# Optimization experiments

Hardware: AMD Instinct MI355X
Metric: run time of the kernel (lower is better)

Reference implementation:

```python
import jax, jax.numpy as jnp
import numpy as np

TOP_K = 2
AUX_COEF = 0.001


def setup_inputs() -> dict:
    key = jax.random.key(0)
    ks = jax.random.split(key, 5)
    B, S, H, I, E = 4, 2048, 1024, 4096, 8
    return {
        "hidden_states": jax.random.normal(ks[0], (B, S, H), dtype=jnp.float32),
        "router_w": jax.random.normal(ks[1], (H, E), dtype=jnp.float32) * 0.02,
        "w_gate": jax.random.normal(ks[2], (E, H, I), dtype=jnp.float32) * 0.02,
        "w_up": jax.random.normal(ks[3], (E, H, I), dtype=jnp.float32) * 0.02,
        "w_down": jax.random.normal(ks[4], (E, I, H), dtype=jnp.float32) * 0.02,
    }


def reference(hidden_states, router_w, w_gate, w_up, w_down):
    B, S, H = hidden_states.shape
    E = router_w.shape[1]
    x = jnp.clip(hidden_states, -10.0, 10.0)          # [B,S,H]
    xf = x.reshape(-1, H)                              # [T,H]
    T = xf.shape[0]

    # --- token-choice router (fp32) ---
    logits = xf.astype(jnp.float32) @ router_w         # [T,E]
    z_loss = jnp.mean(jax.nn.logsumexp(logits, axis=-1) ** 2)
    probs = jax.nn.softmax(logits, axis=-1)            # [T,E]
    top_w, top_i = jax.lax.top_k(probs, TOP_K)         # [T,K]
    top_w = top_w / jnp.sum(top_w, axis=-1, keepdims=True)
    # load-balance loss: aux * E * sum_e f_e * P_e
    assign = jax.nn.one_hot(top_i, E, dtype=jnp.float32).sum(axis=1)  # [T,E]
    frac_tokens = assign.mean(axis=0) / TOP_K
    mean_probs = probs.mean(axis=0)
    lb_loss = AUX_COEF * E * jnp.sum(frac_tokens * mean_probs)

    # --- dense per-expert SwiGLU MLP, then gather selected outputs ---
    expert_outs = []
    for e in range(E):  # small fixed loop over experts
        gate = xf @ w_gate[e]                          # [T,I]
        up = xf @ w_up[e]                              # [T,I]
        expert_outs.append((jax.nn.silu(gate) * up) @ w_down[e])  # [T,H]
    outs = jnp.stack(expert_outs, axis=0)              # [E,T,H]

    gathered = outs[top_i, jnp.arange(T)[:, None], :]  # [T,K,H]
    out = jnp.einsum("tk,tkh->th", top_w.astype(x.dtype), gathered)
    out = jnp.clip(out, -10.0, 10.0).reshape(B, S, H)
    return out, lb_loss, z_loss
```

## Files before the change

kernel.cpp:

```cpp
#include <hip/hip_runtime.h>
#include <stdint.h>

#define TOKENS 8192
#define HDIM 1024
#define IDIM 4096
#define NEXP 8
#define MPAD 17408
#define MTILES 136

typedef float f32x4 __attribute__((ext_vector_type(4)));
typedef __bf16 bf16x8 __attribute__((ext_vector_type(8)));
typedef uint32_t u32x4 __attribute__((ext_vector_type(4)));

static __device__ __forceinline__ uint16_t f2bf(float f) {
  uint32_t u = __builtin_bit_cast(uint32_t, f);
  return (uint16_t)((u + 0x7fffu + ((u >> 16) & 1u)) >> 16);
}
static __device__ __forceinline__ uint32_t pack2(float a, float b) {
  return (uint32_t)f2bf(a) | ((uint32_t)f2bf(b) << 16);
}
static __device__ __forceinline__ float bf2f(uint32_t h) {
  return __builtin_bit_cast(float, h << 16);
}
#define SWZ4(r) (((r) >> 1) & 3u)
static __device__ __forceinline__ void load_lds16(const void* g, void* l) {
  __builtin_amdgcn_global_load_lds(
      (const __attribute__((address_space(1))) uint32_t*)(uintptr_t)g,
      (__attribute__((address_space(3))) uint32_t*)(uintptr_t)l, 16, 0, 0);
}
static __device__ __forceinline__ bf16x8 rdfrag(const char* base, uint32_t row, uint32_t g) {
  return *(const bf16x8*)(base + row * 64 + ((g ^ SWZ4(row)) * 16));
}
static __device__ __forceinline__ void nt_store4(void* p, u32x4 v) {
  __builtin_nontemporal_store(v, (u32x4*)p);
}
#define WAITV(n) asm volatile("s_waitcnt vmcnt(" #n ")" ::: "memory")
#define WAITL0 asm volatile("s_waitcnt lgkmcnt(0)" ::: "memory")
#define BAR __builtin_amdgcn_s_barrier()
#define SCHEDB __builtin_amdgcn_sched_barrier(0)

__global__ __launch_bounds__(256) void router_kernel(
    const float* __restrict__ x, const float* __restrict__ rw,
    uint16_t* __restrict__ xb, float2* __restrict__ topw, int2* __restrict__ tope,
    int* __restrict__ cnt_slots, float* __restrict__ psum_slots, float* __restrict__ zsum_slots) {
  const int tid = threadIdx.x;
  const int lane = tid & 63, wid = tid >> 6;
  const int t = blockIdx.x * 4 + wid;

  const float* xrow = x + (size_t)t * HDIM + lane * 16;
  float xc[16];
#pragma unroll
  for (int i = 0; i < 4; ++i) {
    float4 v = *(const float4*)(xrow + i * 4);
    xc[i * 4 + 0] = fminf(fmaxf(v.x, -10.f), 10.f);
    xc[i * 4 + 1] = fminf(fmaxf(v.y, -10.f), 10.f);
    xc[i * 4 + 2] = fminf(fmaxf(v.z, -10.f), 10.f);
    xc[i * 4 + 3] = fminf(fmaxf(v.w, -10.f), 10.f);
  }
  uint4 o0, o1;
  o0.x = pack2(xc[0], xc[1]);   o0.y = pack2(xc[2], xc[3]);
  o0.z = pack2(xc[4], xc[5]);   o0.w = pack2(xc[6], xc[7]);
  o1.x = pack2(xc[8], xc[9]);   o1.y = pack2(xc[10], xc[11]);
  o1.z = pack2(xc[12], xc[13]); o1.w = pack2(xc[14], xc[15]);
  uint4* dst = (uint4*)(xb + (size_t)t * HDIM + lane * 16);
  dst[0] = o0; dst[1] = o1;

  float acc[8];
#pragma unroll
  for (int e = 0; e < 8; ++e) acc[e] = 0.f;
  const float* rwp = rw + (size_t)(lane * 16) * NEXP;
#pragma unroll
  for (int i = 0; i < 16; ++i) {
    float xi = xc[i];
    float4 a = *(const float4*)(rwp + i * 8);
    float4 b = *(const float4*)(rwp + i * 8 + 4);
    acc[0] += xi * a.x; acc[1] += xi * a.y; acc[2] += xi * a.z; acc[3] += xi * a.w;
    acc[4] += xi * b.x; acc[5] += xi * b.y; acc[6] += xi * b.z; acc[7] += xi * b.w;
  }
#pragma unroll
  for (int s = 1; s < 64; s <<= 1) {
#pragma unroll
    for (int e = 0; e < 8; ++e) acc[e] += __shfl_xor(acc[e], s);
  }

  __shared__ float sp[8]; __shared__ int sc[8]; __shared__ float sz;
  if (tid < 8) { sp[tid] = 0.f; sc[tid] = 0; }
  if (tid == 0) sz = 0.f;
  __syncthreads();

  if (lane == 0) {
    float mx = acc[0];
#pragma unroll
    for (int e = 1; e < 8; ++e) mx = fmaxf(mx, acc[e]);
    float p[8]; float s = 0.f;
#pragma unroll
    for (int e = 0; e < 8; ++e) { p[e] = expf(acc[e] - mx); s += p[e]; }
    float inv = 1.f / s;
#pragma unroll
    for (int e = 0; e < 8; ++e) p[e] *= inv;
    float lse = mx + logf(s);
    int e0 = 0; float b0 = p[0];
#pragma unroll
    for (int e = 1; e < 8; ++e) if (p[e] > b0) { b0 = p[e]; e0 = e; }
    int e1 = (e0 == 0) ? 1 : 0; float b1 = (e0 == 0) ? p[1] : p[0];
#pragma unroll
    for (int e = 0; e < 8; ++e) if (e != e0 && p[e] > b1) { b1 = p[e]; e1 = e; }
    float wn = 1.f / (b0 + b1);
    topw[t] = make_float2(b0 * wn, b1 * wn);
    tope[t] = make_int2(e0, e1);
#pragma unroll
    for (int e = 0; e < 8; ++e) atomicAdd(&sp[e], p[e]);
    atomicAdd(&sc[e0], 1); atomicAdd(&sc[e1], 1);
    atomicAdd(&sz, lse * lse);
  }
  __syncthreads();
  int slot = blockIdx.x & 63;
  if (tid < 8) {
    atomicAdd(&cnt_slots[slot * 8 + tid], sc[tid]);
    atomicAdd(&psum_slots[slot * 8 + tid], sp[tid]);
  }
  if (tid == 0) atomicAdd(&zsum_slots[slot], sz);
}

__global__ void scan_kernel(const int* __restrict__ cnt_slots,
                            const float* __restrict__ psum_slots,
                            const float* __restrict__ zsum_slots,
                            int* __restrict__ seg, int* __restrict__ fill_cnt,
                            float* __restrict__ out_sc) {
  const int tid = threadIdx.x;
  __shared__ int c[8]; __shared__ float ps[8];
  if (tid < 8) {
    int s = 0; float f = 0.f;
    for (int k = 0; k < 64; ++k) { s += cnt_slots[k * 8 + tid]; f += psum_slots[k * 8 + tid]; }
    c[tid] = s; ps[tid] = f; fill_cnt[tid] = 0;
  }
  __syncthreads();
  if (tid == 0) {
    int off = 0;
    for (int e = 0; e < 8; ++e) { seg[e] = off; off += (c[e] + 127) & ~127; }
    seg[8] = off;
    float lb = 0.f;
    for (int e = 0; e < 8; ++e)
      lb += ((float)c[e] / (2.0f * (float)TOKENS)) * (ps[e] / (float)TOKENS);
    lb *= 0.001f * (float)NEXP;
    float z = 0.f;
    for (int k = 0; k < 64; ++k) z += zsum_slots[k];
    out_sc[0] = lb;
    out_sc[1] = z / (float)TOKENS;
  }
}

__global__ __launch_bounds__(256) void fill_kernel(
    const int2* __restrict__ tope, const int* __restrict__ seg,
    int* __restrict__ fill_cnt, int* __restrict__ rowtok) {
  const int t = blockIdx.x * 256 + threadIdx.x;
  const int lane = threadIdx.x & 63;
  const int2 te = tope[t];
#pragma unroll
  for (int k = 0; k < 2; ++k) {
    const int e = k ? te.y : te.x;
    int pos = 0;
    for (int ee = 0; ee < 8; ++ee) {
      unsigned long long mask = __ballot(e == ee);
      if (e == ee) {
        unsigned long long below = mask & ((lane == 0) ? 0ull : (~0ull >> (64 - lane)));
        int nbelow = __popcll(below);
        int leader = __ffsll((unsigned long long)mask) - 1;
        int base = 0;
        if (lane == leader) base = atomicAdd(&fill_cnt[ee], __popcll(mask));
        base = __shfl(base, leader);
        pos = seg[ee] + base + nbelow;
      }
    }
    rowtok[pos] = t * 2 + k;
  }
}

__global__ __launch_bounds__(256) void convert_kernel(
    const float* __restrict__ w_gate, const float* __restrict__ w_up,
    const float* __restrict__ w_down, uint16_t* __restrict__ wgT,
    uint16_t* __restrict__ wuT, uint16_t* __restrict__ wdT) {
  __shared__ uint64_t tt4[4][64][17];
  const int tid = threadIdx.x;
  const int z = blockIdx.y;
  const int bx = blockIdx.x;
  const float* src; uint16_t* dst; int R, C, tr, tq;
  if (z < 16) {
    R = 1024; C = 4096; tr = bx >> 4; tq = bx & 15;
    int e = z & 7;
    src = (z < 8 ? w_gate : w_up) + (size_t)e * 1024 * 4096;
    dst = (z < 8 ? wgT : wuT) + (size_t)e * 1024 * 4096;
  } else {
    R = 4096; C = 1024; tr = bx >> 2; tq = bx & 3;
    int e = z - 16;
    src = w_down + (size_t)e * 4096 * 1024;
    dst = wdT + (size_t)e * 4096 * 1024;
  }
  const int i = tid >> 4, j = tid & 15;
  const float* sb = src + (size_t)(tr * 64 + 4 * i) * C + tq * 256 + 4 * j;
  f32x4 v[4][4];
#pragma unroll
  for (int t4 = 0; t4 < 4; ++t4)
#pragma unroll
    for (int r = 0; r < 4; ++r)
      v[t4][r] = __builtin_nontemporal_load((const f32x4*)(sb + (size_t)r * C + t4 * 64));
#pragma unroll
  for (int t4 = 0; t4 < 4; ++t4)
#pragma unroll
    for (int k = 0; k < 4; ++k)
      tt4[t4][4 * j + k][i] =
          (uint64_t)pack2(v[t4][0][k], v[t4][1][k]) |
          ((uint64_t)pack2(v[t4][2][k], v[t4][3][k]) << 32);
  __syncthreads();
#pragma unroll
  for (int t4 = 0; t4 < 4; ++t4)
#pragma unroll
    for (int it = 0; it < 2; ++it) {
      int idx = it * 256 + tid;
      int c = idx >> 3, h = idx & 7;
      uint64_t a = tt4[t4][c][2 * h], b = tt4[t4][c][2 * h + 1];
      u32x4 w;
      w[0] = (uint32_t)a; w[1] = (uint32_t)(a >> 32);
      w[2] = (uint32_t)b; w[3] = (uint32_t)(b >> 32);
      nt_store4(dst + (size_t)(tq * 256 + t4 * 64 + c) * R + tr * 64 + h * 8, w);
    }
}

static __device__ __forceinline__ int xcd_swz(int b, int nwg) {
  int q = nwg >> 3, r = nwg & 7;
  int xcd = b & 7;
  int base = (xcd < r) ? xcd * (q + 1) : r * (q + 1) + (xcd - r) * q;
  return base + (b >> 3);
}

__global__ __launch_bounds__(256, 2) void gemm1_kernel(
    const uint16_t* __restrict__ xb, const uint16_t* __restrict__ wgT,
    const uint16_t* __restrict__ wuT, const int* __restrict__ rowtok,
    const int* __restrict__ seg, uint16_t* __restrict__ hbuf, int mt0) {
  __shared__ __align__(16) char smem[49152];
  const int tid = threadIdx.x;
  const int lane = tid & 63, wid = tid >> 6;
  const int ct = (int)gridDim.y;
  const int b = (int)(blockIdx.y * gridDim.x + blockIdx.x);
  const int wg_lin = xcd_swz(b, 32 * ct);
  const int iblk = wg_lin / ct;
  const int mrel = wg_lin % ct;
  const int mtile = mt0 + mrel;
  const int row0 = mtile * 128;
  if (row0 >= seg[8]) return;
  int e = 0;
  while (row0 >= seg[e + 1]) ++e;
  const uint16_t* wgp = wgT + (size_t)e * HDIM * IDIM;
  const uint16_t* wup = wuT + (size_t)e * HDIM * IDIM;
  const int icol0 = iblk * 128;

  const uint32_t r0 = (uint32_t)(wid * 32 + (lane >> 2));
  const uint32_t r1 = r0 + 16;
  const uint32_t cc0 = ((lane & 3u) ^ SWZ4(r0)) * 16;
  const uint32_t cc1 = ((lane & 3u) ^ SWZ4(r1)) * 16;
  int rt0 = rowtok[row0 + r0]; int tok0 = (rt0 < 0) ? 0 : (rt0 >> 1);
  int rt1 = rowtok[row0 + r1]; int tok1 = (rt1 < 0) ? 0 : (rt1 >> 1);
  const uintptr_t a0 = (uintptr_t)(xb + (size_t)tok0 * HDIM) + cc0;
  const uintptr_t a1 = (uintptr_t)(xb + (size_t)tok1 * HDIM) + cc1;
  const uintptr_t g0 = (uintptr_t)(wgp + (size_t)(icol0 + r0) * HDIM) + cc0;
  const uintptr_t g1 = (uintptr_t)(wgp + (size_t)(icol0 + r1) * HDIM) + cc1;
  const uintptr_t u0 = (uintptr_t)(wup + (size_t)(icol0 + r0) * HDIM) + cc0;
  const uintptr_t u1 = (uintptr_t)(wup + (size_t)(icol0 + r1) * HDIM) + cc1;
  const uint32_t ldsA = (uint32_t)(wid * 2048);

  f32x4 accg[4][4] = {}; f32x4 accu[4][4] = {};

#define G1_ISSUE(t, buf)                                                        \
  {                                                                             \
    char* B_ = smem + (buf) * 24576;                                            \
    size_t o_ = (size_t)(t) * 64;                                               \
    load_lds16((const void*)(a0 + o_), B_ + ldsA);                              \
    load_lds16((const void*)(a1 + o_), B_ + ldsA + 1024);                       \
    load_lds16((const void*)(g0 + o_), B_ + 8192 + ldsA);                       \
    load_lds16((const void*)(g1 + o_), B_ + 8192 + ldsA + 1024);                \
    load_lds16((const void*)(u0 + o_), B_ + 16384 + ldsA);                      \
    load_lds16((const void*)(u1 + o_), B_ + 16384 + ldsA + 1024);               \
  }

  const uint32_t g = lane >> 4, l15 = lane & 15;
  const uint32_t mrow = (uint32_t)((wid >> 1) * 64) + l15;
  const uint32_t nrow = (uint32_t)((wid & 1) * 64) + l15;

#define G1_PHASE(buf)                                                           \
  {                                                                             \
    const char* B_ = smem + (buf) * 24576;                                      \
    bf16x8 af[4], bg[4], bu[4];                                                 \
    _Pragma("unroll") for (int mi = 0; mi < 4; ++mi)                            \
        af[mi] = rdfrag(B_, mrow + mi * 16, g);                                 \
    _Pragma("unroll") for (int ni = 0; ni < 4; ++ni) {                          \
      bg[ni] = rdfrag(B_ + 8192, nrow + ni * 16, g);                            \
      bu[ni] = rdfrag(B_ + 16384, nrow + ni * 16, g);                           \
    }                                                                           \
    WAITL0; SCHEDB;                                                             \
    BAR; SCHEDB;                                                                \
    ISSUE_NEXT;                                                                 \
    SCHEDB;                                                                     \
    __builtin_amdgcn_s_setprio(1);                                              \
    _Pragma("unroll") for (int mi = 0; mi < 4; ++mi)                            \
        _Pragma("unroll") for (int ni = 0; ni < 4; ++ni) {                      \
      accg[mi][ni] = __builtin_amdgcn_mfma_f32_16x16x32_bf16(af[mi], bg[ni], accg[mi][ni], 0, 0, 0); \
      accu[mi][ni] = __builtin_amdgcn_mfma_f32_16x16x32_bf16(af[mi], bu[ni], accu[mi][ni], 0, 0, 0); \
    }                                                                           \
    __builtin_amdgcn_s_setprio(0);                                              \
  }

  const int NT = HDIM / 32;
  WAITV(0);
  G1_ISSUE(0, 0);
  G1_ISSUE(1, 1);
  for (int t = 0; t < NT - 1; ++t) {
    WAITV(6); BAR; SCHEDB;
#define ISSUE_NEXT if (t + 2 < NT) G1_ISSUE(t + 2, t & 1)
    G1_PHASE(t & 1);
#undef ISSUE_NEXT
  }
  {
    WAITV(0); BAR; SCHEDB;
#define ISSUE_NEXT
    G1_PHASE((NT - 1) & 1);
#undef ISSUE_NEXT
  }

  __syncthreads();
  uint16_t* epi = (uint16_t*)smem;
  const int wr = wid >> 1, wc = wid & 1;
#pragma unroll
  for (int mi = 0; mi < 4; ++mi)
#pragma unroll
    for (int ni = 0; ni < 4; ++ni)
#pragma unroll
      for (int r = 0; r < 4; ++r) {
        float gv = accg[mi][ni][r], uv = accu[mi][ni][r];
        float hv = gv * uv * __frcp_rn(1.0f + __expf(-gv));
        int m = wr * 64 + mi * 16 + (lane >> 4) * 4 + r;
        int n = wc * 64 + ni * 16 + (lane & 15);
        epi[m * 136 + n] = f2bf(hv);
      }
  __syncthreads();
  const int hrow0 = (mtile - mt0) * 128;
  const int m = tid >> 1;
#pragma unroll
  for (int j = 0; j < 8; ++j) {
    int ch = (tid & 1) + j * 2;
    uint4 v = *(const uint4*)(smem + m * 272 + ch * 16);
    *(uint4*)(hbuf + ((size_t)(hrow0 + m)) * IDIM + icol0 + ch * 8) = v;
  }
}

__global__ __launch_bounds__(256, 2) void gemm2_kernel(
    const uint16_t* __restrict__ hbuf, const uint16_t* __restrict__ wdT,
    const int* __restrict__ rowtok, const int* __restrict__ seg,
    uint16_t* __restrict__ pairbuf, int mt0) {
  __shared__ __align__(16) char smem[34816];
  const int tid = threadIdx.x;
  const int lane = tid & 63, wid = tid >> 6;
  const int ct = (int)gridDim.y;
  const int b = (int)(blockIdx.y * gridDim.x + blockIdx.x);
  const int wg_lin = xcd_swz(b, 8 * ct);
  const int nblk = wg_lin / ct;
  const int mrel = wg_lin % ct;
  const int mtile = mt0 + mrel;
  const int row0 = mtile * 128;
  if (row0 >= seg[8]) return;
  int e = 0;
  while (row0 >= seg[e + 1]) ++e;
  const uint16_t* wdp = wdT + (size_t)e * IDIM * HDIM;
  const int ncol0 = nblk * 128;
  const int hrow0 = (mtile - mt0) * 128;

  const uint32_t r0 = (uint32_t)(wid * 32 + (lane >> 2));
  const uint32_t r1 = r0 + 16;
  const uint32_t cc0 = ((lane & 3u) ^ SWZ4(r0)) * 16;
  const uint32_t cc1 = ((lane & 3u) ^ SWZ4(r1)) * 16;
  const uintptr_t a0 = (uintptr_t)(hbuf + (size_t)(hrow0 + r0) * IDIM) + cc0;
  const uintptr_t a1 = (uintptr_t)(hbuf + (size_t)(hrow0 + r1) * IDIM) + cc1;
  const uintptr_t b0 = (uintptr_t)(wdp + (size_t)(ncol0 + r0) * IDIM) + cc0;
  const uintptr_t b1 = (uintptr_t)(wdp + (size_t)(ncol0 + r1) * IDIM) + cc1;
  const uint32_t ldsA = (uint32_t)(wid * 2048);

  f32x4 acc[4][4] = {};

#define G2_ISSUE(t, buf)                                                        \
  {                                                                             \
    char* B_ = smem + (buf) * 16384;                                            \
    size_t o_ = (size_t)(t) * 64;                                               \
    load_lds16((const void*)(a0 + o_), B_ + ldsA);                              \
    load_lds16((const void*)(a1 + o_), B_ + ldsA + 1024);                       \
    load_lds16((const void*)(b0 + o_), B_ + 8192 + ldsA);                       \
    load_lds16((const void*)(b1 + o_), B_ + 8192 + ldsA + 1024);                \
  }

  const uint32_t g = lane >> 4, l15 = lane & 15;
  const uint32_t mrow = (uint32_t)((wid >> 1) * 64) + l15;
  const uint32_t nrow = (uint32_t)((wid & 1) * 64) + l15;

#define G2_PHASE(buf)                                                           \
  {                                                                             \
    const char* B_ = smem + (buf) * 16384;                                      \
    bf16x8 af[4], bf[4];                                                        \
    _Pragma("unroll") for (int mi = 0; mi < 4; ++mi)                            \
        af[mi] = rdfrag(B_, mrow + mi * 16, g);                                 \
    _Pragma("unroll") for (int ni = 0; ni < 4; ++ni)                            \
        bf[ni] = rdfrag(B_ + 8192, nrow + ni * 16, g);                          \
    WAITL0; SCHEDB;                                                             \
    BAR; SCHEDB;                                                                \
    ISSUE_NEXT;                                                                 \
    SCHEDB;                                                                     \
    __builtin_amdgcn_s_setprio(1);                                              \
    _Pragma("unroll") for (int mi = 0; mi < 4; ++mi)                            \
        _Pragma("unroll") for (int ni = 0; ni < 4; ++ni)                        \
            acc[mi][ni] = __builtin_amdgcn_mfma_f32_16x16x32_bf16(af[mi], bf[ni], acc[mi][ni], 0, 0, 0); \
    __builtin_amdgcn_s_setprio(0);                                              \
  }

  const int NT = IDIM / 32;
  WAITV(0);
  G2_ISSUE(0, 0);
  G2_ISSUE(1, 1);
  for (int t = 0; t < NT - 1; ++t) {
    WAITV(4); BAR; SCHEDB;
#define ISSUE_NEXT if (t + 2 < NT) G2_ISSUE(t + 2, t & 1)
    G2_PHASE(t & 1);
#undef ISSUE_NEXT
  }
  {
    WAITV(0); BAR; SCHEDB;
#define ISSUE_NEXT
    G2_PHASE((NT - 1) & 1);
#undef ISSUE_NEXT
  }

  __syncthreads();
  uint16_t* epi = (uint16_t*)smem;
  const int wr = wid >> 1, wc = wid & 1;
#pragma unroll
  for (int mi = 0; mi < 4; ++mi)
#pragma unroll
    for (int ni = 0; ni < 4; ++ni)
#pragma unroll
      for (int r = 0; r < 4; ++r) {
        int m = wr * 64 + mi * 16 + (lane >> 4) * 4 + r;
        int n = wc * 64 + ni * 16 + (lane & 15);
        epi[m * 136 + n] = f2bf(acc[mi][ni][r]);
      }
  __syncthreads();
  const int m = tid >> 1;
  const int rt = rowtok[row0 + m];
  if (rt >= 0) {
#pragma unroll
    for (int j = 0; j < 8; ++j) {
      int ch = (tid & 1) + j * 2;
      uint4 v = *(const uint4*)(smem + m * 272 + ch * 16);
      *(uint4*)(pairbuf + (size_t)rt * HDIM + ncol0 + ch * 8) = v;
    }
  }
}

__global__ __launch_bounds__(256) void combine_kernel(
    const uint16_t* __restrict__ pairbuf, const float2* __restrict__ topw,
    float* __restrict__ out) {
  size_t i = (size_t)blockIdx.x * 256 + threadIdx.x;
  int t = (int)(i >> 7);
  int ch = (int)(i & 127);
  float2 w = topw[t];
  const uint16_t* p0 = pairbuf + (size_t)(t * 2) * HDIM + ch * 8;
  uint4 a = *(const uint4*)p0;
  uint4 b = *(const uint4*)(p0 + HDIM);
  float o[8];
  uint32_t au[4] = {a.x, a.y, a.z, a.w};
  uint32_t bu[4] = {b.x, b.y, b.z, b.w};
#pragma unroll
  for (int j = 0; j < 4; ++j) {
    float v0 = w.x * bf2f(au[j] & 0xffffu) + w.y * bf2f(bu[j] & 0xffffu);
    float v1 = w.x * bf2f(au[j] >> 16) + w.y * bf2f(bu[j] >> 16);
    o[j * 2 + 0] = fminf(fmaxf(v0, -10.f), 10.f);
    o[j * 2 + 1] = fminf(fmaxf(v1, -10.f), 10.f);
  }
  float* op = out + (size_t)t * HDIM + ch * 8;
  float4 w0 = {o[0], o[1], o[2], o[3]};
  float4 w1 = {o[4], o[5], o[6], o[7]};
  *(float4*)op = w0;
  *(float4*)(op + 4) = w1;
}

extern "C" void kernel_launch(void* const* d_in, const int* in_sizes, int n_in,
                              void* d_out, int out_size, void* d_ws, size_t ws_size,
                              hipStream_t stream) {
  (void)in_sizes; (void)n_in; (void)out_size;
  const float* x = (const float*)d_in[0];
  const float* rw = (const float*)d_in[1];
  const float* w_gate = (const float*)d_in[2];
  const float* w_up = (const float*)d_in[3];
  const float* w_down = (const float*)d_in[4];
  float* out = (float*)d_out;

  char* ws = (char*)d_ws;
  size_t off = 0;
  auto alloc = [&](size_t n) { char* p = ws + off; off += (n + 255) & ~(size_t)255; return p; };
  uint16_t* xb = (uint16_t*)alloc((size_t)TOKENS * HDIM * 2);
  float2* topw = (float2*)alloc((size_t)TOKENS * 8);
  int2* tope = (int2*)alloc((size_t)TOKENS * 8);
  int* rowtok = (int*)alloc((size_t)MPAD * 4);
  int* seg = (int*)alloc(16 * 4);
  int* fill_cnt = (int*)alloc(8 * 4);
  int* cnt_slots = (int*)alloc(64 * 8 * 4);
  float* psum_slots = (float*)alloc(64 * 8 * 4);
  float* zsum_slots = (float*)alloc(64 * 4);
  uint16_t* pairbuf = (uint16_t*)alloc((size_t)TOKENS * 2 * HDIM * 2);
  uint16_t* wgT = (uint16_t*)alloc((size_t)NEXP * HDIM * IDIM * 2);
  uint16_t* wuT = (uint16_t*)alloc((size_t)NEXP * HDIM * IDIM * 2);
  uint16_t* wdT = (uint16_t*)alloc((size_t)NEXP * IDIM * HDIM * 2);
  uint16_t* hbuf = (uint16_t*)(ws + off);
  size_t avail = (ws_size > off) ? (ws_size - off) : 0;
  long tiles_fit = (long)(avail / (128ull * IDIM * 2));
  int chunk = (tiles_fit >= MTILES) ? MTILES : (tiles_fit < 1 ? 1 : (int)tiles_fit);

  hipMemsetAsync(cnt_slots, 0, 64 * 8 * 4, stream);
  hipMemsetAsync(psum_slots, 0, 64 * 8 * 4, stream);
  hipMemsetAsync(zsum_slots, 0, 64 * 4, stream);
  hipMemsetAsync(rowtok, 0xFF, (size_t)MPAD * 4, stream);

  convert_kernel<<<dim3(256, 24), 256, 0, stream>>>(w_gate, w_up, w_down, wgT, wuT, wdT);
  router_kernel<<<TOKENS / 4, 256, 0, stream>>>(x, rw, xb, topw, tope,
                                                cnt_slots, psum_slots, zsum_slots);
  scan_kernel<<<1, 64, 0, stream>>>(cnt_slots, psum_slots, zsum_slots, seg, fill_cnt,
                                    out + (size_t)TOKENS * HDIM);
  fill_kernel<<<TOKENS / 256, 256, 0, stream>>>(tope, seg, fill_cnt, rowtok);

  for (int mt0 = 0; mt0 < MTILES; mt0 += chunk) {
    int ct = (MTILES - mt0 < chunk) ? (MTILES - mt0) : chunk;
    gemm1_kernel<<<dim3(IDIM / 128, ct), 256, 0, stream>>>(xb, wgT, wuT, rowtok, seg, hbuf, mt0);
    gemm2_kernel<<<dim3(HDIM / 128, ct), 256, 0, stream>>>(hbuf, wdT, rowtok, seg, pairbuf, mt0);
  }
  combine_kernel<<<(TOKENS * HDIM / 8) / 256, 256, 0, stream>>>(pairbuf, topw, out);
}
```

Before: 710.3 us.

## Double-buffer LDS fragments in registers to overlap reads with MFMA

Restructures both grouped GEMM main loops so the LDS-to-register fragment reads for the next K-step are issued before the MFMAs of the current step, using two register fragment sets that alternate across an unrolled-by-two loop. The goal is to hide LDS read latency behind matrix-core work instead of waiting on lgkmcnt before every MFMA block. The sched_barrier fences are removed, which leaves instruction interleaving to the compiler. The extra fragment registers raise VGPR pressure, and the barrier placement around the reuse of the two LDS buffers has changed, which could add stalls or create hazards.

```diff
diff --git a/kernel.cpp b/kernel.cpp
--- a/kernel.cpp
+++ b/kernel.cpp
@@ -37,7 +37,6 @@
 #define WAITV(n) asm volatile("s_waitcnt vmcnt(" #n ")" ::: "memory")
 #define WAITL0 asm volatile("s_waitcnt lgkmcnt(0)" ::: "memory")
 #define BAR __builtin_amdgcn_s_barrier()
-#define SCHEDB __builtin_amdgcn_sched_barrier(0)
 
 __global__ __launch_bounds__(256) void router_kernel(
     const float* __restrict__ x, const float* __restrict__ rw,
@@ -269,6 +268,7 @@
   const uint32_t ldsA = (uint32_t)(wid * 2048);
 
   f32x4 accg[4][4] = {}; f32x4 accu[4][4] = {};
+  bf16x8 af0[4], bg0[4], bu0[4], af1[4], bg1[4], bu1[4];
 
 #define G1_ISSUE(t, buf)                                                        \
   {                                                                             \
@@ -286,25 +286,24 @@
   const uint32_t mrow = (uint32_t)((wid >> 1) * 64) + l15;
   const uint32_t nrow = (uint32_t)((wid & 1) * 64) + l15;
 
-#define G1_PHASE(buf)                                                           \
+#define G1_READ(buf, AF, BG, BU)                                                \
   {                                                                             \
     const char* B_ = smem + (buf) * 24576;                                      \
-    bf16x8 af[4], bg[4], bu[4];                                                 \
     _Pragma("unroll") for (int mi = 0; mi < 4; ++mi)                            \
-        af[mi] = rdfrag(B_, mrow + mi * 16, g);                                 \
+        AF[mi] = rdfrag(B_, mrow + mi * 16, g);                                 \
     _Pragma("unroll") for (int ni = 0; ni < 4; ++ni) {                          \
-      bg[ni] = rdfrag(B_ + 8192, nrow + ni * 16, g);                            \
-      bu[ni] = rdfrag(B_ + 16384, nrow + ni * 16, g);                           \
+      BG[ni] = rdfrag(B_ + 8192, nrow + ni * 16, g);                            \
+      BU[ni] = rdfrag(B_ + 16384, nrow + ni * 16, g);                           \
     }                                                                           \
-    WAITL0; SCHEDB;                                                             \
-    BAR; SCHEDB;                                                                \
-    ISSUE_NEXT;                                                                 \
-    SCHEDB;                                                                     \
+  }
+
+#define G1_MFMA(AF, BG, BU)                                                     \
+  {                                                                             \
     __builtin_amdgcn_s_setprio(1);                                              \
     _Pragma("unroll") for (int mi = 0; mi < 4; ++mi)                            \
         _Pragma("unroll") for (int ni = 0; ni < 4; ++ni) {                      \
-      accg[mi][ni] = __builtin_amdgcn_mfma_f32_16x16x32_bf16(af[mi], bg[ni], accg[mi][ni], 0, 0, 0); \
-      accu[mi][ni] = __builtin_amdgcn_mfma_f32_16x16x32_bf16(af[mi], bu[ni], accu[mi][ni], 0, 0, 0); \
+      accg[mi][ni] = __builtin_amdgcn_mfma_f32_16x16x32_bf16(AF[mi], BG[ni], accg[mi][ni], 0, 0, 0); \
+      accu[mi][ni] = __builtin_amdgcn_mfma_f32_16x16x32_bf16(AF[mi], BU[ni], accu[mi][ni], 0, 0, 0); \
     }                                                                           \
     __builtin_amdgcn_s_setprio(0);                                              \
   }
@@ -313,18 +312,23 @@
   WAITV(0);
   G1_ISSUE(0, 0);
   G1_ISSUE(1, 1);
-  for (int t = 0; t < NT - 1; ++t) {
-    WAITV(6); BAR; SCHEDB;
-#define ISSUE_NEXT if (t + 2 < NT) G1_ISSUE(t + 2, t & 1)
-    G1_PHASE(t & 1);
-#undef ISSUE_NEXT
-  }
-  {
-    WAITV(0); BAR; SCHEDB;
-#define ISSUE_NEXT
-    G1_PHASE((NT - 1) & 1);
-#undef ISSUE_NEXT
-  }
+  WAITV(6); BAR;
+  G1_READ(0, af0, bg0, bu0);
+  for (int t = 0; t <= NT - 4; t += 2) {
+    G1_ISSUE(t + 2, 0); WAITV(6); BAR;
+    G1_READ(1, af1, bg1, bu1);
+    G1_MFMA(af0, bg0, bu0);
+    WAITL0; BAR;
+    G1_ISSUE(t + 3, 1); WAITV(6); BAR;
+    G1_READ(0, af0, bg0, bu0);
+    G1_MFMA(af1, bg1, bu1);
+    WAITL0; BAR;
+  }
+  WAITV(0); BAR;
+  G1_READ(1, af1, bg1, bu1);
+  G1_MFMA(af0, bg0, bu0);
+  WAITL0; BAR;
+  G1_MFMA(af1, bg1, bu1);
 
   __syncthreads();
   uint16_t* epi = (uint16_t*)smem;
@@ -384,6 +388,7 @@
   const uint32_t ldsA = (uint32_t)(wid * 2048);
 
   f32x4 acc[4][4] = {};
+  bf16x8 af0[4], bf0[4], af1[4], bf1[4];
 
 #define G2_ISSUE(t, buf)                                                        \
   {                                                                             \
@@ -399,22 +404,21 @@
   const uint32_t mrow = (uint32_t)((wid >> 1) * 64) + l15;
   const uint32_t nrow = (uint32_t)((wid & 1) * 64) + l15;
 
-#define G2_PHASE(buf)                                                           \
+#define G2_READ(buf, AF, BF)                                                    \
   {                                                                             \
     const char* B_ = smem + (buf) * 16384;                                      \
-    bf16x8 af[4], bf[4];                                                        \
     _Pragma("unroll") for (int mi = 0; mi < 4; ++mi)                            \
-        af[mi] = rdfrag(B_, mrow + mi * 16, g);                                 \
+        AF[mi] = rdfrag(B_, mrow + mi * 16, g);                                 \
     _Pragma("unroll") for (int ni = 0; ni < 4; ++ni)                            \
-        bf[ni] = rdfrag(B_ + 8192, nrow + ni * 16, g);                          \
-    WAITL0; SCHEDB;                                                             \
-    BAR; SCHEDB;                                                                \
-    ISSUE_NEXT;                                                                 \
-    SCHEDB;                                                                     \
+        BF[ni] = rdfrag(B_ + 8192, nrow + ni * 16, g);                          \
+  }
+
+#define G2_MFMA(AF, BF)                                                         \
+  {                                                                             \
     __builtin_amdgcn_s_setprio(1);                                              \
     _Pragma("unroll") for (int mi = 0; mi < 4; ++mi)                            \
         _Pragma("unroll") for (int ni = 0; ni < 4; ++ni)                        \
-            acc[mi][ni] = __builtin_amdgcn_mfma_f32_16x16x32_bf16(af[mi], bf[ni], acc[mi][ni], 0, 0, 0); \
+            acc[mi][ni] = __builtin_amdgcn_mfma_f32_16x16x32_bf16(AF[mi], BF[ni], acc[mi][ni], 0, 0, 0); \
     __builtin_amdgcn_s_setprio(0);                                              \
   }
 
@@ -422,18 +426,23 @@
   WAITV(0);
   G2_ISSUE(0, 0);
   G2_ISSUE(1, 1);
-  for (int t = 0; t < NT - 1; ++t) {
-    WAITV(4); BAR; SCHEDB;
-#define ISSUE_NEXT if (t + 2 < NT) G2_ISSUE(t + 2, t & 1)
-    G2_PHASE(t & 1);
-#undef ISSUE_NEXT
-  }
-  {
-    WAITV(0); BAR; SCHEDB;
-#define ISSUE_NEXT
-    G2_PHASE((NT - 1) & 1);
-#undef ISSUE_NEXT
-  }
+  WAITV(4); BAR;
+  G2_READ(0, af0, bf0);
+  for (int t = 0; t <= NT - 4; t += 2) {
+    G2_ISSUE(t + 2, 0); WAITV(4); BAR;
+    G2_READ(1, af1, bf1);
+    G2_MFMA(af0, bf0);
+    WAITL0; BAR;
+    G2_ISSUE(t + 3, 1); WAITV(4); BAR;
+    G2_READ(0, af0, bf0);
+    G2_MFMA(af1, bf1);
+    WAITL0; BAR;
+  }
+  WAITV(0); BAR;
+  G2_READ(1, af1, bf1);
+  G2_MFMA(af0, bf0);
+  WAITL0; BAR;
+  G2_MFMA(af1, bf1);
 
   __syncthreads();
   uint16_t* epi = (uint16_t*)smem;
```

Result: slower. 730.6 us (+2.8%).

## Retile gate/up GEMM to 256x128 tiles with 8 waves and K-step 64

Applied to the files above, without the earlier changes.

The gate/up grouped GEMM now computes 256-row by 128-column tiles with 512 threads, loading 64-wide K slices into a 128 KB double-buffered LDS. It uses a new XOR swizzle and a phased MFMA schedule with barriers and priority boosts. Expert segments are padded to multiples of 256, and the down-projection GEMM is launched with twice as many 128-row tiles to match. The goal is more reuse of each weight tile and fewer iterations per tile. In exchange, the larger padding adds wasted rows, the large LDS footprint limits residency to one block per CU, and the extra barriers may serialize the waves.

```diff
diff --git a/kernel.cpp b/kernel.cpp
--- a/kernel.cpp
+++ b/kernel.cpp
@@ -5,8 +5,8 @@
 #define HDIM 1024
 #define IDIM 4096
 #define NEXP 8
-#define MPAD 17408
-#define MTILES 136
+#define MPAD 18432
+#define MT256 72
 
 typedef float f32x4 __attribute__((ext_vector_type(4)));
 typedef __bf16 bf16x8 __attribute__((ext_vector_type(8)));
@@ -37,7 +37,9 @@
 #define WAITV(n) asm volatile("s_waitcnt vmcnt(" #n ")" ::: "memory")
 #define WAITL0 asm volatile("s_waitcnt lgkmcnt(0)" ::: "memory")
 #define BAR __builtin_amdgcn_s_barrier()
-#define SCHEDB __builtin_amdgcn_sched_barrier(0)
+#define PRIO1 __builtin_amdgcn_s_setprio(1)
+#define PRIO0 __builtin_amdgcn_s_setprio(0)
+#define MM(d, a, b) d = __builtin_amdgcn_mfma_f32_16x16x32_bf16(a, b, d, 0, 0, 0)
 
 __global__ __launch_bounds__(256) void router_kernel(
     const float* __restrict__ x, const float* __restrict__ rw,
@@ -137,7 +139,7 @@
   __syncthreads();
   if (tid == 0) {
     int off = 0;
-    for (int e = 0; e < 8; ++e) { seg[e] = off; off += (c[e] + 127) & ~127; }
+    for (int e = 0; e < 8; ++e) { seg[e] = off; off += (c[e] + 255) & ~255; }
     seg[8] = off;
     float lb = 0.f;
     for (int e = 0; e < 8; ++e)
@@ -233,11 +235,12 @@
   return base + (b >> 3);
 }
 
-__global__ __launch_bounds__(256, 2) void gemm1_kernel(
+#define NT_G1 16
+__global__ __launch_bounds__(512, 2) void gemm1_kernel(
     const uint16_t* __restrict__ xb, const uint16_t* __restrict__ wgT,
     const uint16_t* __restrict__ wuT, const int* __restrict__ rowtok,
     const int* __restrict__ seg, uint16_t* __restrict__ hbuf, int mt0) {
-  __shared__ __align__(16) char smem[49152];
+  __shared__ __align__(16) char smem[131072];
   const int tid = threadIdx.x;
   const int lane = tid & 63, wid = tid >> 6;
   const int ct = (int)gridDim.y;
@@ -246,7 +249,7 @@
   const int iblk = wg_lin / ct;
   const int mrel = wg_lin % ct;
   const int mtile = mt0 + mrel;
-  const int row0 = mtile * 128;
+  const int row0 = mtile * 256;
   if (row0 >= seg[8]) return;
   int e = 0;
   while (row0 >= seg[e + 1]) ++e;
@@ -254,101 +257,119 @@
   const uint16_t* wup = wuT + (size_t)e * HDIM * IDIM;
   const int icol0 = iblk * 128;
 
-  const uint32_t r0 = (uint32_t)(wid * 32 + (lane >> 2));
-  const uint32_t r1 = r0 + 16;
-  const uint32_t cc0 = ((lane & 3u) ^ SWZ4(r0)) * 16;
-  const uint32_t cc1 = ((lane & 3u) ^ SWZ4(r1)) * 16;
-  int rt0 = rowtok[row0 + r0]; int tok0 = (rt0 < 0) ? 0 : (rt0 >> 1);
-  int rt1 = rowtok[row0 + r1]; int tok1 = (rt1 < 0) ? 0 : (rt1 >> 1);
-  const uintptr_t a0 = (uintptr_t)(xb + (size_t)tok0 * HDIM) + cc0;
-  const uintptr_t a1 = (uintptr_t)(xb + (size_t)tok1 * HDIM) + cc1;
-  const uintptr_t g0 = (uintptr_t)(wgp + (size_t)(icol0 + r0) * HDIM) + cc0;
-  const uintptr_t g1 = (uintptr_t)(wgp + (size_t)(icol0 + r1) * HDIM) + cc1;
-  const uintptr_t u0 = (uintptr_t)(wup + (size_t)(icol0 + r0) * HDIM) + cc0;
-  const uintptr_t u1 = (uintptr_t)(wup + (size_t)(icol0 + r1) * HDIM) + cc1;
-  const uint32_t ldsA = (uint32_t)(wid * 2048);
-
-  f32x4 accg[4][4] = {}; f32x4 accu[4][4] = {};
+  const uint32_t csrc = (((uint32_t)lane & 7u) ^ ((uint32_t)lane >> 3)) * 16u;
+  uintptr_t aS[4];
+#pragma unroll
+  for (int j = 0; j < 4; ++j) {
+    uint32_t r = (uint32_t)((wid * 4 + j) * 8 + (lane >> 3));
+    int rt = rowtok[row0 + r]; int tok = (rt < 0) ? 0 : (rt >> 1);
+    aS[j] = (uintptr_t)(xb + (size_t)tok * HDIM) + csrc;
+  }
+  uintptr_t gS[2], uS[2];
+#pragma unroll
+  for (int j = 0; j < 2; ++j) {
+    uint32_t n = (uint32_t)((wid * 2 + j) * 8 + (lane >> 3));
+    gS[j] = (uintptr_t)(wgp + (size_t)(icol0 + n) * HDIM) + csrc;
+    uS[j] = (uintptr_t)(wup + (size_t)(icol0 + n) * HDIM) + csrc;
+  }
+  const uint32_t ldsAj = (uint32_t)(wid * 4096);
+  const uint32_t ldsBj = (uint32_t)(wid * 2048);
 
 #define G1_ISSUE(t, buf)                                                        \
   {                                                                             \
-    char* B_ = smem + (buf) * 24576;                                            \
-    size_t o_ = (size_t)(t) * 64;                                               \
-    load_lds16((const void*)(a0 + o_), B_ + ldsA);                              \
-    load_lds16((const void*)(a1 + o_), B_ + ldsA + 1024);                       \
-    load_lds16((const void*)(g0 + o_), B_ + 8192 + ldsA);                       \
-    load_lds16((const void*)(g1 + o_), B_ + 8192 + ldsA + 1024);                \
-    load_lds16((const void*)(u0 + o_), B_ + 16384 + ldsA);                      \
-    load_lds16((const void*)(u1 + o_), B_ + 16384 + ldsA + 1024);               \
+    size_t o_ = (size_t)(t) * 128;                                              \
+    char* A_ = smem + (buf) * 32768;                                            \
+    char* G_ = smem + 65536 + (buf) * 16384;                                    \
+    char* U_ = smem + 98304 + (buf) * 16384;                                    \
+    load_lds16((const void*)(aS[0] + o_), A_ + ldsAj);                          \
+    load_lds16((const void*)(aS[1] + o_), A_ + ldsAj + 1024);                   \
+    load_lds16((const void*)(aS[2] + o_), A_ + ldsAj + 2048);                   \
+    load_lds16((const void*)(aS[3] + o_), A_ + ldsAj + 3072);                   \
+    load_lds16((const void*)(gS[0] + o_), G_ + ldsBj);                          \
+    load_lds16((const void*)(gS[1] + o_), G_ + ldsBj + 1024);                   \
+    load_lds16((const void*)(uS[0] + o_), U_ + ldsBj);                          \
+    load_lds16((const void*)(uS[1] + o_), U_ + ldsBj + 1024);                   \
   }
 
   const uint32_t g = lane >> 4, l15 = lane & 15;
-  const uint32_t mrow = (uint32_t)((wid >> 1) * 64) + l15;
-  const uint32_t nrow = (uint32_t)((wid & 1) * 64) + l15;
-
-#define G1_PHASE(buf)                                                           \
+  const int wm = wid >> 2, wn = wid & 3;
+  const uint32_t arow0 = (uint32_t)(wm * 128) + l15;
+  const uint32_t brow0 = (uint32_t)(wn * 32) + l15;
+  const uint32_t sw0 = (g ^ (l15 & 7u)) * 16u;
+  const uint32_t sw1 = ((4u | g) ^ (l15 & 7u)) * 16u;
+
+#define RDA(buf, mi, kk) (*(const bf16x8*)(smem + (buf) * 32768 + (arow0 + (mi) * 16) * 128 + ((kk) ? sw1 : sw0)))
+#define RDG(buf, ni, kk) (*(const bf16x8*)(smem + 65536 + (buf) * 16384 + (brow0 + (ni) * 16) * 128 + ((kk) ? sw1 : sw0)))
+#define RDU(buf, ni, kk) (*(const bf16x8*)(smem + 98304 + (buf) * 16384 + (brow0 + (ni) * 16) * 128 + ((kk) ? sw1 : sw0)))
+
+  f32x4 accg[8][2] = {}; f32x4 accu[8][2] = {};
+
+#define G1_MFMA_P(p)                                                            \
+  MM(accg[2*(p)][0], a00, Bg00); MM(accg[2*(p)][1], a00, Bg10);                 \
+  MM(accu[2*(p)][0], a00, Bu00); MM(accu[2*(p)][1], a00, Bu10);                 \
+  MM(accg[2*(p)+1][0], a10, Bg00); MM(accg[2*(p)+1][1], a10, Bg10);             \
+  MM(accu[2*(p)+1][0], a10, Bu00); MM(accu[2*(p)+1][1], a10, Bu10);             \
+  MM(accg[2*(p)][0], a01, Bg01); MM(accg[2*(p)][1], a01, Bg11);                 \
+  MM(accu[2*(p)][0], a01, Bu01); MM(accu[2*(p)][1], a01, Bu11);                 \
+  MM(accg[2*(p)+1][0], a11, Bg01); MM(accg[2*(p)+1][1], a11, Bg11);             \
+  MM(accu[2*(p)+1][0], a11, Bu01); MM(accu[2*(p)+1][1], a11, Bu11);
+
+#define G1_PH(buf, p)                                                           \
   {                                                                             \
-    const char* B_ = smem + (buf) * 24576;                                      \
-    bf16x8 af[4], bg[4], bu[4];                                                 \
-    _Pragma("unroll") for (int mi = 0; mi < 4; ++mi)                            \
-        af[mi] = rdfrag(B_, mrow + mi * 16, g);                                 \
-    _Pragma("unroll") for (int ni = 0; ni < 4; ++ni) {                          \
-      bg[ni] = rdfrag(B_ + 8192, nrow + ni * 16, g);                            \
-      bu[ni] = rdfrag(B_ + 16384, nrow + ni * 16, g);                           \
+    bf16x8 a00 = RDA(buf, 2*(p), 0), a01 = RDA(buf, 2*(p), 1);                  \
+    bf16x8 a10 = RDA(buf, 2*(p)+1, 0), a11 = RDA(buf, 2*(p)+1, 1);              \
+    BAR; WAITL0;                                                                \
+    PRIO1; G1_MFMA_P(p); PRIO0; BAR;                                            \
+  }
+
+#define G1_TILE(buf, tt)                                                        \
+  {                                                                             \
+    bf16x8 Bg00 = RDG(buf,0,0), Bg01 = RDG(buf,0,1), Bg10 = RDG(buf,1,0), Bg11 = RDG(buf,1,1); \
+    bf16x8 Bu00 = RDU(buf,0,0), Bu01 = RDU(buf,0,1), Bu10 = RDU(buf,1,0), Bu11 = RDU(buf,1,1); \
+    G1_PH(buf, 0)                                                               \
+    G1_PH(buf, 1)                                                               \
+    G1_PH(buf, 2)                                                               \
+    {                                                                           \
+      bf16x8 a00 = RDA(buf, 6, 0), a01 = RDA(buf, 6, 1);                        \
+      bf16x8 a10 = RDA(buf, 7, 0), a11 = RDA(buf, 7, 1);                        \
+      BAR; WAITL0;                                                              \
+      PRIO1; G1_MFMA_P(3); PRIO0; BAR;                                          \
+      if ((tt) + 2 < NT_G1) { G1_ISSUE((tt) + 2, buf); WAITV(8); }              \
+      else { WAITV(0); }                                                        \
+      BAR;                                                                      \
     }                                                                           \
-    WAITL0; SCHEDB;                                                             \
-    BAR; SCHEDB;                                                                \
-    ISSUE_NEXT;                                                                 \
-    SCHEDB;                                                                     \
-    __builtin_amdgcn_s_setprio(1);                                              \
-    _Pragma("unroll") for (int mi = 0; mi < 4; ++mi)                            \
-        _Pragma("unroll") for (int ni = 0; ni < 4; ++ni) {                      \
-      accg[mi][ni] = __builtin_amdgcn_mfma_f32_16x16x32_bf16(af[mi], bg[ni], accg[mi][ni], 0, 0, 0); \
-      accu[mi][ni] = __builtin_amdgcn_mfma_f32_16x16x32_bf16(af[mi], bu[ni], accu[mi][ni], 0, 0, 0); \
-    }                                                                           \
-    __builtin_amdgcn_s_setprio(0);                                              \
-  }
-
-  const int NT = HDIM / 32;
+  }
+
   WAITV(0);
   G1_ISSUE(0, 0);
   G1_ISSUE(1, 1);
-  for (int t = 0; t < NT - 1; ++t) {
-    WAITV(6); BAR; SCHEDB;
-#define ISSUE_NEXT if (t + 2 < NT) G1_ISSUE(t + 2, t & 1)
-    G1_PHASE(t & 1);
-#undef ISSUE_NEXT
-  }
-  {
-    WAITV(0); BAR; SCHEDB;
-#define ISSUE_NEXT
-    G1_PHASE((NT - 1) & 1);
-#undef ISSUE_NEXT
+  WAITV(8); BAR;
+  for (int t = 0; t < NT_G1; t += 2) {
+    G1_TILE(0, t)
+    G1_TILE(1, t + 1)
   }
 
   __syncthreads();
   uint16_t* epi = (uint16_t*)smem;
-  const int wr = wid >> 1, wc = wid & 1;
-#pragma unroll
-  for (int mi = 0; mi < 4; ++mi)
-#pragma unroll
-    for (int ni = 0; ni < 4; ++ni)
+#pragma unroll
+  for (int mi = 0; mi < 8; ++mi)
+#pragma unroll
+    for (int ni = 0; ni < 2; ++ni)
 #pragma unroll
       for (int r = 0; r < 4; ++r) {
         float gv = accg[mi][ni][r], uv = accu[mi][ni][r];
         float hv = gv * uv * __frcp_rn(1.0f + __expf(-gv));
-        int m = wr * 64 + mi * 16 + (lane >> 4) * 4 + r;
-        int n = wc * 64 + ni * 16 + (lane & 15);
+        int m = wm * 128 + mi * 16 + (lane >> 4) * 4 + r;
+        int n = wn * 32 + ni * 16 + l15;
         epi[m * 136 + n] = f2bf(hv);
       }
   __syncthreads();
-  const int hrow0 = (mtile - mt0) * 128;
-  const int m = tid >> 1;
+  const int hrow0 = (mtile - mt0) * 256;
+  const int m = tid >> 1, half = tid & 1;
 #pragma unroll
   for (int j = 0; j < 8; ++j) {
-    int ch = (tid & 1) + j * 2;
-    uint4 v = *(const uint4*)(smem + m * 272 + ch * 16);
-    *(uint4*)(hbuf + ((size_t)(hrow0 + m)) * IDIM + icol0 + ch * 8) = v;
+    uint4 v = *(const uint4*)(epi + m * 136 + half * 64 + j * 8);
+    *(uint4*)(hbuf + (size_t)(hrow0 + m) * IDIM + icol0 + half * 64 + j * 8) = v;
   }
 }
 
@@ -407,15 +428,17 @@
         af[mi] = rdfrag(B_, mrow + mi * 16, g);                                 \
     _Pragma("unroll") for (int ni = 0; ni < 4; ++ni)                            \
         bf[ni] = rdfrag(B_ + 8192, nrow + ni * 16, g);                          \
-    WAITL0; SCHEDB;                                                             \
-    BAR; SCHEDB;                                                                \
+    WAITL0;                                                                     \
+    __builtin_amdgcn_sched_barrier(0);                                          \
+    BAR;                                                                        \
+    __builtin_amdgcn_sched_barrier(0);                                          \
     ISSUE_NEXT;                                                                 \
-    SCHEDB;                                                                     \
-    __builtin_amdgcn_s_setprio(1);                                              \
+    __builtin_amdgcn_sched_barrier(0);                                          \
+    PRIO1;                                                                      \
     _Pragma("unroll") for (int mi = 0; mi < 4; ++mi)                            \
         _Pragma("unroll") for (int ni = 0; ni < 4; ++ni)                        \
             acc[mi][ni] = __builtin_amdgcn_mfma_f32_16x16x32_bf16(af[mi], bf[ni], acc[mi][ni], 0, 0, 0); \
-    __builtin_amdgcn_s_setprio(0);                                              \
+    PRIO0;                                                                      \
   }
 
   const int NT = IDIM / 32;
@@ -423,13 +446,13 @@
   G2_ISSUE(0, 0);
   G2_ISSUE(1, 1);
   for (int t = 0; t < NT - 1; ++t) {
-    WAITV(4); BAR; SCHEDB;
+    WAITV(4); BAR; __builtin_amdgcn_sched_barrier(0);
 #define ISSUE_NEXT if (t + 2 < NT) G2_ISSUE(t + 2, t & 1)
     G2_PHASE(t & 1);
 #undef ISSUE_NEXT
   }
   {
-    WAITV(0); BAR; SCHEDB;
+    WAITV(0); BAR; __builtin_amdgcn_sched_barrier(0);
 #define ISSUE_NEXT
     G2_PHASE((NT - 1) & 1);
 #undef ISSUE_NEXT
@@ -517,8 +540,8 @@
   uint16_t* wdT = (uint16_t*)alloc((size_t)NEXP * IDIM * HDIM * 2);
   uint16_t* hbuf = (uint16_t*)(ws + off);
   size_t avail = (ws_size > off) ? (ws_size - off) : 0;
-  long tiles_fit = (long)(avail / (128ull * IDIM * 2));
-  int chunk = (tiles_fit >= MTILES) ? MTILES : (tiles_fit < 1 ? 1 : (int)tiles_fit);
+  long fit256 = (long)(avail / (256ull * IDIM * 2));
+  int chunk256 = (fit256 >= MT256) ? MT256 : (fit256 < 1 ? 1 : (int)fit256);
 
   hipMemsetAsync(cnt_slots, 0, 64 * 8 * 4, stream);
   hipMemsetAsync(psum_slots, 0, 64 * 8 * 4, stream);
@@ -532,10 +555,10 @@
                                     out + (size_t)TOKENS * HDIM);
   fill_kernel<<<TOKENS / 256, 256, 0, stream>>>(tope, seg, fill_cnt, rowtok);
 
-  for (int mt0 = 0; mt0 < MTILES; mt0 += chunk) {
-    int ct = (MTILES - mt0 < chunk) ? (MTILES - mt0) : chunk;
-    gemm1_kernel<<<dim3(IDIM / 128, ct), 256, 0, stream>>>(xb, wgT, wuT, rowtok, seg, hbuf, mt0);
-    gemm2_kernel<<<dim3(HDIM / 128, ct), 256, 0, stream>>>(hbuf, wdT, rowtok, seg, pairbuf, mt0);
+  for (int mt0 = 0; mt0 < MT256; mt0 += chunk256) {
+    int ct = (MT256 - mt0 < chunk256) ? (MT256 - mt0) : chunk256;
+    gemm1_kernel<<<dim3(IDIM / 128, ct), 512, 0, stream>>>(xb, wgT, wuT, rowtok, seg, hbuf, mt0);
+    gemm2_kernel<<<dim3(HDIM / 128, 2 * ct), 256, 0, stream>>>(hbuf, wdT, rowtok, seg, pairbuf, 2 * mt0);
   }
   combine_kernel<<<(TOKENS * HDIM / 8) / 256, 256, 0, stream>>>(pairbuf, topw, out);
 }
```

Result: slower. 769.6 us (+8.3%).
